# Kernel optimization log

Hardware: AMD Instinct MI355X
Metric: run time of the kernel (lower is better)

## Reference

```python
import jax, jax.numpy as jnp
import numpy as np

NHEADS = 16
NGROUPS = 16
NEG = -1e9

def _apply_rope(t, cos, sin):
    # t: (B,T,H,hs) -> pairs (B,T,H,hs//2,2); complex multiply by (cos + i*sin)
    B, T, H, hs = t.shape
    tp = t.reshape(B, T, H, hs // 2, 2)
    a, b = tp[..., 0], tp[..., 1]
    c = cos[None, :, None, :]
    s = sin[None, :, None, :]
    out = jnp.stack([a * c - b * s, a * s + b * c], axis=-1)
    return out.reshape(B, T, H, hs)

def _causal_attn(q, k, v):
    # q,k: (..., S, d); v: (..., S, dv); causal softmax attention, scale 1/sqrt(d)
    d = q.shape[-1]
    S = q.shape[-2]
    scores = jnp.einsum('...qd,...kd->...qk', q, k) / jnp.sqrt(jnp.asarray(d, q.dtype))
    mask = jnp.tril(jnp.ones((S, S), dtype=bool))
    scores = jnp.where(mask, scores, NEG)
    p = jax.nn.softmax(scores, axis=-1)
    return jnp.einsum('...qk,...kd->...qd', p, v)

def setup_inputs() -> dict:
    key = jax.random.key(0)
    k1, k2, k3 = jax.random.split(key, 3)
    B, T, C = 4, 2048, 1024
    hs = C // NHEADS
    x = jax.random.normal(k1, (B, T, C), dtype=jnp.float32)
    w_attn = jax.random.normal(k2, (3 * C, C), dtype=jnp.float32) * (1.0 / np.sqrt(C))
    w_proj = jax.random.normal(k3, (C, C), dtype=jnp.float32) * (1.0 / np.sqrt(C))
    # standard RoPE frequencies: theta_i = 10000^{-2i/hs}
    inv = 1.0 / (10000.0 ** (np.arange(0, hs, 2, dtype=np.float32) / hs))  # (hs//2,)
    ang = np.arange(T, dtype=np.float32)[:, None] * inv[None, :]           # (T, hs//2)
    freqs_cos = jnp.asarray(np.cos(ang), dtype=jnp.float32)
    freqs_sin = jnp.asarray(np.sin(ang), dtype=jnp.float32)
    return {'x': x, 'w_attn': w_attn, 'w_proj': w_proj,
            'freqs_cos': freqs_cos, 'freqs_sin': freqs_sin}

def reference(x, w_attn, w_proj, freqs_cos, freqs_sin):
    B, T, C = x.shape
    H = NHEADS
    hs = C // H
    G = min(T // (T // NGROUPS), NGROUPS)  # group_t = block_size // ngroups, T == block_size
    Tg = T // G
    qkv = x @ w_attn.T                      # (B,T,3C)
    q, k, v = jnp.split(qkv, 3, axis=2)
    # RoPE
    q = _apply_rope(q.reshape(B, T, H, hs), freqs_cos, freqs_sin).reshape(B, T, C)
    k = _apply_rope(k.reshape(B, T, H, hs), freqs_cos, freqs_sin).reshape(B, T, C)
    # group: (B, G, Tg, H, hs) -> (B, H, G, Tg, hs)
    def grp(t):
        return t.reshape(B, G, Tg, H, hs).transpose(0, 3, 1, 2, 4)
    q, k, v = grp(q), grp(k), grp(v)
    # its_time branch: append mean-pooled summary token per group
    q = jnp.concatenate([q, q.mean(axis=3, keepdims=True)], axis=3)  # (B,H,G,Tg+1,hs)
    k = jnp.concatenate([k, k.mean(axis=3, keepdims=True)], axis=3)
    v = jnp.concatenate([v, v.mean(axis=3, keepdims=True)], axis=3)
    att = _causal_attn(q, k, v)             # (B,H,G,Tg+1,hs)
    # group-level attention over summary tokens of all but last group
    q2 = q[:, :, :-1, -1]                   # (B,H,G-1,hs)
    k2 = k[:, :, :-1, -1]
    av = att[:, :, :-1, -1]                 # (B,H,G-1,hs)
    v2 = _causal_attn(q2, k2, av)           # (B,H,G-1,hs)
    y_q = q2[:, :, :, None, :]              # (B,H,G-1,1,hs)
    y_k = k2[:, :, :, None, :]
    y_v = v2[:, :, :, None, :]
    # drop summary tokens, merge groups back: (B,H,G,Tg,hs) -> (B,T,C)
    xo = att[:, :, :, :-1]
    xo = xo.reshape(B, H, T, hs).transpose(0, 2, 1, 3).reshape(B, T, C)
    out = xo @ w_proj.T
    return (out, y_q, y_k, y_v)
```

## Files before the change

kernel.cpp:

```cpp
#include <hip/hip_runtime.h>
#include <hip/hip_bf16.h>

#define HS 64
#define NH 16
#define NG 16
#define TT 2048
#define CC 1024
#define BBATCH 4
#define TG 128
#define SS 129

typedef __attribute__((ext_vector_type(8))) short bf16x8;
typedef __attribute__((ext_vector_type(4))) float f32x4;

__device__ __forceinline__ float bf2f(ushort u) {
  return __uint_as_float(((unsigned)u) << 16);
}
__device__ __forceinline__ ushort f2bf(float f) {
  unsigned x = __float_as_uint(f);
  x += 0x7fff + ((x >> 16) & 1);
  return (ushort)(x >> 16);
}
__device__ __forceinline__ bf16x8 mk8(ushort4 a0, ushort4 a1) {
  bf16x8 v;
  v[0] = (short)a0.x; v[1] = (short)a0.y; v[2] = (short)a0.z; v[3] = (short)a0.w;
  v[4] = (short)a1.x; v[5] = (short)a1.y; v[6] = (short)a1.z; v[7] = (short)a1.w;
  return v;
}

__global__ void cvt3(const float* __restrict__ x, const float* __restrict__ wa,
                     const float* __restrict__ wp, ushort* __restrict__ xb,
                     ushort* __restrict__ wab, ushort* __restrict__ wpb) {
  const int stride = gridDim.x * blockDim.x;
  for (int i = blockIdx.x * blockDim.x + threadIdx.x; i < 3145728; i += stride) {
    const float* src; ushort* dst; int off;
    if (i < 2097152) { src = x; dst = xb; off = i; }
    else if (i < 2883584) { src = wa; dst = wab; off = i - 2097152; }
    else { src = wp; dst = wpb; off = i - 2883584; }
    float4 v = ((const float4*)src)[off];
    ushort4 o;
    o.x = f2bf(v.x); o.y = f2bf(v.y); o.z = f2bf(v.z); o.w = f2bf(v.w);
    ((ushort4*)dst)[off] = o;
  }
}

__global__ __launch_bounds__(512) void gemm_qkv3(const ushort* __restrict__ A,
                                                 const ushort* __restrict__ Bw,
                                                 ushort* __restrict__ Cout) {
  const int Kd = 1024, Nd = 3072;
  __shared__ ushort As[128][68];
  __shared__ ushort Bs[384][68];
  const int m0 = blockIdx.y * 128;
  const int n0 = blockIdx.x * 384;
  const int tid = threadIdx.x;
  const int lane = tid & 63;
  const int wv = tid >> 6;
  const int wm = wv >> 2, wn = wv & 3;
  const int lo = lane & 15, hi = lane >> 4;
  const int rb = tid >> 3;
  const int c8 = (tid & 7) * 8;

  f32x4 acc[4][6];
#pragma unroll
  for (int i = 0; i < 4; ++i)
#pragma unroll
    for (int j = 0; j < 6; ++j) acc[i][j] = (f32x4)0.0f;

  uint4 v0, v1, v2, v3, v4, v5, v6, v7;
#define LOADQ(k0_)                                                              \
  {                                                                             \
    v0 = *(const uint4*)(A + (size_t)(m0 + rb) * Kd + (k0_) + c8);              \
    v1 = *(const uint4*)(A + (size_t)(m0 + rb + 64) * Kd + (k0_) + c8);         \
    v2 = *(const uint4*)(Bw + (size_t)(n0 + rb) * Kd + (k0_) + c8);             \
    v3 = *(const uint4*)(Bw + (size_t)(n0 + rb + 64) * Kd + (k0_) + c8);        \
    v4 = *(const uint4*)(Bw + (size_t)(n0 + rb + 128) * Kd + (k0_) + c8);       \
    v5 = *(const uint4*)(Bw + (size_t)(n0 + rb + 192) * Kd + (k0_) + c8);       \
    v6 = *(const uint4*)(Bw + (size_t)(n0 + rb + 256) * Kd + (k0_) + c8);       \
    v7 = *(const uint4*)(Bw + (size_t)(n0 + rb + 320) * Kd + (k0_) + c8);       \
  }
#define STOREQ                                                                  \
  {                                                                             \
    *(uint2*)&As[rb][c8]            = make_uint2(v0.x, v0.y);                   \
    *(uint2*)&As[rb][c8 + 4]        = make_uint2(v0.z, v0.w);                   \
    *(uint2*)&As[rb + 64][c8]       = make_uint2(v1.x, v1.y);                   \
    *(uint2*)&As[rb + 64][c8 + 4]   = make_uint2(v1.z, v1.w);                   \
    *(uint2*)&Bs[rb][c8]            = make_uint2(v2.x, v2.y);                   \
    *(uint2*)&Bs[rb][c8 + 4]        = make_uint2(v2.z, v2.w);                   \
    *(uint2*)&Bs[rb + 64][c8]       = make_uint2(v3.x, v3.y);                   \
    *(uint2*)&Bs[rb + 64][c8 + 4]   = make_uint2(v3.z, v3.w);                   \
    *(uint2*)&Bs[rb + 128][c8]      = make_uint2(v4.x, v4.y);                   \
    *(uint2*)&Bs[rb + 128][c8 + 4]  = make_uint2(v4.z, v4.w);                   \
    *(uint2*)&Bs[rb + 192][c8]      = make_uint2(v5.x, v5.y);                   \
    *(uint2*)&Bs[rb + 192][c8 + 4]  = make_uint2(v5.z, v5.w);                   \
    *(uint2*)&Bs[rb + 256][c8]      = make_uint2(v6.x, v6.y);                   \
    *(uint2*)&Bs[rb + 256][c8 + 4]  = make_uint2(v6.z, v6.w);                   \
    *(uint2*)&Bs[rb + 320][c8]      = make_uint2(v7.x, v7.y);                   \
    *(uint2*)&Bs[rb + 320][c8 + 4]  = make_uint2(v7.z, v7.w);                   \
  }

  LOADQ(0)
  for (int t = 0; t < 16; ++t) {
    __syncthreads();
    STOREQ
    __syncthreads();
    if (t < 15) LOADQ((t + 1) * 64)
#pragma unroll
    for (int kk = 0; kk < 64; kk += 32) {
      bf16x8 af[4], bfr[6];
#pragma unroll
      for (int i = 0; i < 4; ++i) {
        int r = wm * 64 + i * 16 + lo;
        af[i] = mk8(*(const ushort4*)&As[r][kk + 4 * hi],
                    *(const ushort4*)&As[r][kk + 16 + 4 * hi]);
      }
#pragma unroll
      for (int j = 0; j < 6; ++j) {
        int r = wn * 96 + j * 16 + lo;
        bfr[j] = mk8(*(const ushort4*)&Bs[r][kk + 4 * hi],
                     *(const ushort4*)&Bs[r][kk + 16 + 4 * hi]);
      }
#pragma unroll
      for (int i = 0; i < 4; ++i)
#pragma unroll
        for (int j = 0; j < 6; ++j)
          acc[i][j] = __builtin_amdgcn_mfma_f32_16x16x32_bf16(af[i], bfr[j], acc[i][j], 0, 0, 0);
    }
  }
#undef LOADQ
#undef STOREQ

#pragma unroll
  for (int i = 0; i < 4; ++i) {
    int row = m0 + wm * 64 + i * 16 + 4 * hi;
#pragma unroll
    for (int j = 0; j < 6; ++j) {
      int col = n0 + wn * 96 + j * 16 + lo;
#pragma unroll
      for (int r = 0; r < 4; ++r)
        Cout[(size_t)(row + r) * Nd + col] = f2bf(acc[i][j][r]);
    }
  }
}

template <bool OUT_BF16>
__global__ __launch_bounds__(256) void gemm_bt(const ushort* __restrict__ A,
                                               const ushort* __restrict__ Bw,
                                               void* __restrict__ Cout,
                                               int M, int N, int K) {
  __shared__ ushort As[128][68];
  __shared__ ushort Bs[128][68];
  const int m0 = blockIdx.y * 128;
  const int n0 = blockIdx.x * 128;
  const int tid = threadIdx.x;
  const int lane = tid & 63;
  const int wv = tid >> 6;
  const int wr = wv >> 1, wc = wv & 1;
  const int lo = lane & 15, hi = lane >> 4;

  f32x4 acc[4][4];
#pragma unroll
  for (int i = 0; i < 4; ++i)
#pragma unroll
    for (int j = 0; j < 4; ++j) acc[i][j] = (f32x4)0.0f;

  for (int k0 = 0; k0 < K; k0 += 64) {
    __syncthreads();
#pragma unroll
    for (int t = 0; t < 4; ++t) {
      int c = tid + 256 * t;
      int row = c >> 3, cc = c & 7;
      uint4 va = *(const uint4*)(A + (size_t)(m0 + row) * K + k0 + cc * 8);
      *(uint2*)&As[row][cc * 8]     = make_uint2(va.x, va.y);
      *(uint2*)&As[row][cc * 8 + 4] = make_uint2(va.z, va.w);
      uint4 vb = *(const uint4*)(Bw + (size_t)(n0 + row) * K + k0 + cc * 8);
      *(uint2*)&Bs[row][cc * 8]     = make_uint2(vb.x, vb.y);
      *(uint2*)&Bs[row][cc * 8 + 4] = make_uint2(vb.z, vb.w);
    }
    __syncthreads();
#pragma unroll
    for (int kk = 0; kk < 64; kk += 32) {
      bf16x8 af[4], bfr[4];
#pragma unroll
      for (int i = 0; i < 4; ++i) {
        int r = wr * 64 + i * 16 + lo;
        af[i] = mk8(*(const ushort4*)&As[r][kk + 4 * hi],
                    *(const ushort4*)&As[r][kk + 16 + 4 * hi]);
      }
#pragma unroll
      for (int j = 0; j < 4; ++j) {
        int r = wc * 64 + j * 16 + lo;
        bfr[j] = mk8(*(const ushort4*)&Bs[r][kk + 4 * hi],
                     *(const ushort4*)&Bs[r][kk + 16 + 4 * hi]);
      }
#pragma unroll
      for (int i = 0; i < 4; ++i)
#pragma unroll
        for (int j = 0; j < 4; ++j)
          acc[i][j] = __builtin_amdgcn_mfma_f32_16x16x32_bf16(af[i], bfr[j], acc[i][j], 0, 0, 0);
    }
  }
#pragma unroll
  for (int i = 0; i < 4; ++i) {
    int row = m0 + wr * 64 + i * 16 + 4 * hi;
#pragma unroll
    for (int j = 0; j < 4; ++j) {
      int col = n0 + wc * 64 + j * 16 + lo;
#pragma unroll
      for (int r = 0; r < 4; ++r) {
        float v = acc[i][j][r];
        if constexpr (OUT_BF16) {
          ((ushort*)Cout)[(size_t)(row + r) * N + col] = f2bf(v);
        } else {
          ((float*)Cout)[(size_t)(row + r) * N + col] = v;
        }
      }
    }
  }
}

__global__ __launch_bounds__(512, 4) void attn1f(const ushort* __restrict__ qkv,
                                                 const float* __restrict__ fc,
                                                 const float* __restrict__ fs,
                                                 ushort* __restrict__ xo, float* __restrict__ attm,
                                                 float* __restrict__ yq, float* __restrict__ yk) {
  __shared__ ushort qs[144][68];
  __shared__ ushort ks[144][68];
  __shared__ ushort vt[64][148];
  __shared__ ushort obuf[8][16][68];
  float (*redL)[8][24] = reinterpret_cast<float(*)[8][24]>(&obuf[0][0][0]);
  const int blk = blockIdx.x;
  const int g = blk & 15, h = (blk >> 4) & 15, b = blk >> 8;
  const int tid = threadIdx.x;
  const int lane = tid & 63, wv = tid >> 6;
  const int lo = lane & 15, hi = lane >> 4;

  if (tid < 320) {
    int d = tid / 5, ch = (tid % 5) * 4;
    *(ushort4*)&vt[d][128 + ch] = make_ushort4(0, 0, 0, 0);
  }

  const size_t rowbase = (size_t)(b * TT + g * TG) * (3 * CC) + h * HS;
  const int srow = tid >> 3;
  const int c8 = (tid & 7) * 8;
  float msq[8], msk[8], msv[8];
#pragma unroll
  for (int j = 0; j < 8; ++j) { msq[j] = 0.f; msk[j] = 0.f; msv[j] = 0.f; }
#pragma unroll
  for (int it = 0; it < 6; ++it) {
    const int part = it >> 1;
    const int s = srow + 64 * (it & 1);
    uint4 w = *(const uint4*)(qkv + rowbase + (size_t)s * (3 * CC) + part * CC + c8);
    ushort e[8];
    *(uint4*)e = w;
    if (part == 2) {
#pragma unroll
      for (int j = 0; j < 8; ++j) { msv[j] += bf2f(e[j]); vt[c8 + j][s] = e[j]; }
    } else {
      const int ts = g * TG + s;
      float4 cv = *(const float4*)&fc[ts * 32 + (c8 >> 1)];
      float4 sv = *(const float4*)&fs[ts * 32 + (c8 >> 1)];
      float a0 = bf2f(e[0]), a1 = bf2f(e[1]), a2 = bf2f(e[2]), a3 = bf2f(e[3]);
      float a4 = bf2f(e[4]), a5 = bf2f(e[5]), a6 = bf2f(e[6]), a7 = bf2f(e[7]);
      float r0 = a0 * cv.x - a1 * sv.x, r1 = a0 * sv.x + a1 * cv.x;
      float r2 = a2 * cv.y - a3 * sv.y, r3 = a2 * sv.y + a3 * cv.y;
      float r4 = a4 * cv.z - a5 * sv.z, r5 = a4 * sv.z + a5 * cv.z;
      float r6 = a6 * cv.w - a7 * sv.w, r7 = a6 * sv.w + a7 * cv.w;
      uint4 o;
      o.x = (unsigned)f2bf(r0) | ((unsigned)f2bf(r1) << 16);
      o.y = (unsigned)f2bf(r2) | ((unsigned)f2bf(r3) << 16);
      o.z = (unsigned)f2bf(r4) | ((unsigned)f2bf(r5) << 16);
      o.w = (unsigned)f2bf(r6) | ((unsigned)f2bf(r7) << 16);
      if (part == 0) {
        *(uint4*)&qs[s][c8] = o;
        msq[0] += r0; msq[1] += r1; msq[2] += r2; msq[3] += r3;
        msq[4] += r4; msq[5] += r5; msq[6] += r6; msq[7] += r7;
      } else {
        *(uint4*)&ks[s][c8] = o;
        msk[0] += r0; msk[1] += r1; msk[2] += r2; msk[3] += r3;
        msk[4] += r4; msk[5] += r5; msk[6] += r6; msk[7] += r7;
      }
    }
  }
#pragma unroll
  for (int j = 0; j < 8; ++j) {
    msq[j] += __shfl_xor(msq[j], 8); msq[j] += __shfl_xor(msq[j], 16); msq[j] += __shfl_xor(msq[j], 32);
    msk[j] += __shfl_xor(msk[j], 8); msk[j] += __shfl_xor(msk[j], 16); msk[j] += __shfl_xor(msk[j], 32);
    msv[j] += __shfl_xor(msv[j], 8); msv[j] += __shfl_xor(msv[j], 16); msv[j] += __shfl_xor(msv[j], 32);
  }
  if (lane < 8) {
#pragma unroll
    for (int j = 0; j < 8; ++j) {
      redL[wv][lane][j] = msq[j];
      redL[wv][lane][8 + j] = msk[j];
      redL[wv][lane][16 + j] = msv[j];
    }
  }
  __syncthreads();
  if (tid < 64) {
    const int cg = tid >> 3, j = tid & 7;
    float mq = 0.f, mk2 = 0.f, mv = 0.f;
#pragma unroll
    for (int w = 0; w < 8; ++w) {
      mq += redL[w][cg][j];
      mk2 += redL[w][cg][8 + j];
      mv += redL[w][cg][16 + j];
    }
    mq *= (1.0f / 128.0f); mk2 *= (1.0f / 128.0f); mv *= (1.0f / 128.0f);
    qs[128][tid] = f2bf(mq);
    ks[128][tid] = f2bf(mk2);
    vt[tid][128] = f2bf(mv);
    if (g < 15) {
      size_t yo = ((size_t)(b * 16 + h) * 15 + g) * 64 + tid;
      yq[yo] = mq; yk[yo] = mk2;
    }
  }
  __syncthreads();

#pragma unroll
  for (int ti = 0; ti < 2; ++ti) {
    const int t = (ti == 0) ? (8 - wv) : ((wv == 7) ? 0 : -1);
    if (t < 0) continue;
    const int q0 = t * 16;

    bf16x8 bq[2];
#pragma unroll
    for (int k2 = 0; k2 < 2; ++k2)
      bq[k2] = mk8(*(const ushort4*)&qs[q0 + lo][k2 * 32 + 4 * hi],
                   *(const ushort4*)&qs[q0 + lo][k2 * 32 + 16 + 4 * hi]);

    f32x4 sc[9];
#pragma unroll
    for (int n = 0; n < 9; ++n) sc[n] = (f32x4)0.0f;
#pragma unroll
    for (int n = 0; n < 9; ++n) {
      if (n > t) continue;
#pragma unroll
      for (int k2 = 0; k2 < 2; ++k2) {
        bf16x8 ak = mk8(*(const ushort4*)&ks[n * 16 + lo][k2 * 32 + 4 * hi],
                        *(const ushort4*)&ks[n * 16 + lo][k2 * 32 + 16 + 4 * hi]);
        sc[n] = __builtin_amdgcn_mfma_f32_16x16x32_bf16(ak, bq[k2], sc[n], 0, 0, 0);
      }
    }

    const int qi = q0 + lo;
    float mx = -INFINITY;
#pragma unroll
    for (int n = 0; n < 9; ++n) {
      if (n > t) continue;
#pragma unroll
      for (int r = 0; r < 4; ++r) {
        int kj = n * 16 + 4 * hi + r;
        float v = (kj <= qi) ? sc[n][r] * 0.125f : -INFINITY;
        sc[n][r] = v;
        mx = fmaxf(mx, v);
      }
    }
    mx = fmaxf(mx, __shfl_xor(mx, 16));
    mx = fmaxf(mx, __shfl_xor(mx, 32));
    float sum = 0.f;
#pragma unroll
    for (int n = 0; n < 9; ++n) {
      if (n > t) continue;
#pragma unroll
      for (int r = 0; r < 4; ++r) {
        float e = __expf(sc[n][r] - mx);
        sc[n][r] = e;
        sum += e;
      }
    }
    sum += __shfl_xor(sum, 16);
    sum += __shfl_xor(sum, 32);
    const float inv = 1.0f / sum;

    f32x4 oac[4];
#pragma unroll
    for (int m = 0; m < 4; ++m) oac[m] = (f32x4)0.0f;
#pragma unroll
    for (int s2 = 0; s2 < 5; ++s2) {
      if (s2 > (t >> 1)) continue;
      const int kt1ok = (2 * s2 + 1 <= t);
      bf16x8 pb;
#pragma unroll
      for (int e = 0; e < 4; ++e) pb[e] = (short)f2bf(sc[2 * s2][e] * inv);
      if (kt1ok) {
#pragma unroll
        for (int e = 0; e < 4; ++e) pb[e + 4] = (short)f2bf(sc[2 * s2 + 1][e] * inv);
      } else {
#pragma unroll
        for (int e = 0; e < 4; ++e) pb[e + 4] = 0;
      }
#pragma unroll
      for (int m = 0; m < 4; ++m) {
        ushort4 a0 = *(const ushort4*)&vt[m * 16 + lo][32 * s2 + 4 * hi];
        ushort4 a1 = kt1ok ? *(const ushort4*)&vt[m * 16 + lo][32 * s2 + 16 + 4 * hi]
                           : make_ushort4(0, 0, 0, 0);
        oac[m] = __builtin_amdgcn_mfma_f32_16x16x32_bf16(mk8(a0, a1), pb, oac[m], 0, 0, 0);
      }
    }

    if (t < 8) {
#pragma unroll
      for (int m = 0; m < 4; ++m)
#pragma unroll
        for (int r = 0; r < 4; ++r)
          obuf[wv][lo][m * 16 + 4 * hi + r] = f2bf(oac[m][r]);
#pragma unroll
      for (int it = 0; it < 4; ++it) {
        int idx = lane + 64 * it;
        int r = idx >> 4;
        int c4 = (idx & 15) * 4;
        uint2 val = *(const uint2*)&obuf[wv][r][c4];
        int tok = g * TG + t * 16 + r;
        *(uint2*)(xo + ((size_t)(b * TT + tok)) * CC + h * HS + c4) = val;
      }
    } else {
      if (lo == 0) {
#pragma unroll
        for (int m = 0; m < 4; ++m)
#pragma unroll
          for (int r = 0; r < 4; ++r)
            attm[(size_t)blk * 64 + m * 16 + 4 * hi + r] = oac[m][r];
      }
    }
  }
}

__global__ __launch_bounds__(64) void attn2(const float* __restrict__ yq,
                                            const float* __restrict__ yk,
                                            const float* __restrict__ attm,
                                            float* __restrict__ yv) {
  __shared__ float qs2[15][64], ks2[15][64], avs[15][64], srow[16];
  int bh = blockIdx.x, lane = threadIdx.x;
  for (int j = 0; j < 15; ++j) {
    qs2[j][lane] = yq[((size_t)bh * 15 + j) * 64 + lane];
    ks2[j][lane] = yk[((size_t)bh * 15 + j) * 64 + lane];
    avs[j][lane] = attm[((size_t)bh * 16 + j) * 64 + lane];
  }
  __syncthreads();
  for (int i = 0; i < 15; ++i) {
    float qv = qs2[i][lane];
    for (int j = 0; j <= i; ++j) {
      float t = qv * ks2[j][lane];
#pragma unroll
      for (int off = 32; off > 0; off >>= 1) t += __shfl_xor(t, off);
      if (lane == 0) srow[j] = t * 0.125f;
    }
    __syncthreads();
    float mx = -INFINITY;
    for (int j = 0; j <= i; ++j) mx = fmaxf(mx, srow[j]);
    float den = 0;
    for (int j = 0; j <= i; ++j) den += __expf(srow[j] - mx);
    float inv = 1.0f / den;
    float o = 0;
    for (int j = 0; j <= i; ++j) o += __expf(srow[j] - mx) * inv * avs[j][lane];
    yv[((size_t)bh * 15 + i) * 64 + lane] = o;
    __syncthreads();
  }
}

extern "C" void kernel_launch(void* const* d_in, const int* in_sizes, int n_in,
                              void* d_out, int out_size, void* d_ws, size_t ws_size,
                              hipStream_t stream) {
  const float* x      = (const float*)d_in[0];
  const float* w_attn = (const float*)d_in[1];
  const float* w_proj = (const float*)d_in[2];
  const float* fc     = (const float*)d_in[3];
  const float* fs     = (const float*)d_in[4];
  float* out = (float*)d_out;

  char* ws = (char*)d_ws;
  ushort* xb   = (ushort*)(ws);
  ushort* xo   = (ushort*)(ws);
  ushort* wab  = (ushort*)(ws + 16777216);
  float*  attm = (float*) (ws + 16777216);
  ushort* wpb  = (ushort*)(ws + 23068672);
  ushort* qkv  = (ushort*)(ws + 25165824);

  float* yq = out + 8388608;
  float* yk = out + 8450048;
  float* yv = out + 8511488;

  cvt3<<<2048, 256, 0, stream>>>(x, w_attn, w_proj, xb, wab, wpb);
  gemm_qkv3<<<dim3(8, 64), 512, 0, stream>>>(xb, wab, qkv);
  attn1f<<<1024, 512, 0, stream>>>(qkv, fc, fs, xo, attm, yq, yk);
  attn2<<<64, 64, 0, stream>>>(yq, yk, attm, yv);
  gemm_bt<false><<<dim3(8, 64), 256, 0, stream>>>(xo, wpb, out, 8192, 1024, 1024);
}
```

Baseline: 179.5 us.

## Drop Q and output LDS buffers in attn1f to raise occupancy

The q shared tile is removed: each wave re-reads its own query rows from global qkv and applies RoPE in registers right before the QK MFMA. Only the mean summary row stays in a small shared buffer. The output staging buffer is also removed, so results go straight from accumulators to global memory as ushort4 stores. The V padding is reduced and the launch-bounds occupancy hint rises from 4 to 6 blocks. The aim is to cut LDS use per block so more blocks fit per CU, at the cost of a second global read of Q with RoPE recomputed and less coalesced output writes.

```diff
diff --git a/kernel.cpp b/kernel.cpp
--- a/kernel.cpp
+++ b/kernel.cpp
@@ -218,25 +218,24 @@
   }
 }
 
-__global__ __launch_bounds__(512, 4) void attn1f(const ushort* __restrict__ qkv,
+__global__ __launch_bounds__(512, 6) void attn1f(const ushort* __restrict__ qkv,
                                                  const float* __restrict__ fc,
                                                  const float* __restrict__ fs,
                                                  ushort* __restrict__ xo, float* __restrict__ attm,
                                                  float* __restrict__ yq, float* __restrict__ yk) {
-  __shared__ ushort qs[144][68];
   __shared__ ushort ks[144][68];
-  __shared__ ushort vt[64][148];
-  __shared__ ushort obuf[8][16][68];
-  float (*redL)[8][24] = reinterpret_cast<float(*)[8][24]>(&obuf[0][0][0]);
+  __shared__ ushort vt[64][144];
+  __shared__ float redL[8][8][24];
+  __shared__ ushort mqrow[64];
   const int blk = blockIdx.x;
   const int g = blk & 15, h = (blk >> 4) & 15, b = blk >> 8;
   const int tid = threadIdx.x;
   const int lane = tid & 63, wv = tid >> 6;
   const int lo = lane & 15, hi = lane >> 4;
 
-  if (tid < 320) {
-    int d = tid / 5, ch = (tid % 5) * 4;
-    *(ushort4*)&vt[d][128 + ch] = make_ushort4(0, 0, 0, 0);
+  if (tid < 256) {
+    int d = tid >> 2, c4 = 128 + (tid & 3) * 4;
+    *(ushort4*)&vt[d][c4] = make_ushort4(0, 0, 0, 0);
   }
 
   const size_t rowbase = (size_t)(b * TT + g * TG) * (3 * CC) + h * HS;
@@ -265,16 +264,15 @@
       float r2 = a2 * cv.y - a3 * sv.y, r3 = a2 * sv.y + a3 * cv.y;
       float r4 = a4 * cv.z - a5 * sv.z, r5 = a4 * sv.z + a5 * cv.z;
       float r6 = a6 * cv.w - a7 * sv.w, r7 = a6 * sv.w + a7 * cv.w;
-      uint4 o;
-      o.x = (unsigned)f2bf(r0) | ((unsigned)f2bf(r1) << 16);
-      o.y = (unsigned)f2bf(r2) | ((unsigned)f2bf(r3) << 16);
-      o.z = (unsigned)f2bf(r4) | ((unsigned)f2bf(r5) << 16);
-      o.w = (unsigned)f2bf(r6) | ((unsigned)f2bf(r7) << 16);
       if (part == 0) {
-        *(uint4*)&qs[s][c8] = o;
         msq[0] += r0; msq[1] += r1; msq[2] += r2; msq[3] += r3;
         msq[4] += r4; msq[5] += r5; msq[6] += r6; msq[7] += r7;
       } else {
+        uint4 o;
+        o.x = (unsigned)f2bf(r0) | ((unsigned)f2bf(r1) << 16);
+        o.y = (unsigned)f2bf(r2) | ((unsigned)f2bf(r3) << 16);
+        o.z = (unsigned)f2bf(r4) | ((unsigned)f2bf(r5) << 16);
+        o.w = (unsigned)f2bf(r6) | ((unsigned)f2bf(r7) << 16);
         *(uint4*)&ks[s][c8] = o;
         msk[0] += r0; msk[1] += r1; msk[2] += r2; msk[3] += r3;
         msk[4] += r4; msk[5] += r5; msk[6] += r6; msk[7] += r7;
@@ -306,7 +304,7 @@
       mv += redL[w][cg][16 + j];
     }
     mq *= (1.0f / 128.0f); mk2 *= (1.0f / 128.0f); mv *= (1.0f / 128.0f);
-    qs[128][tid] = f2bf(mq);
+    mqrow[tid] = f2bf(mq);
     ks[128][tid] = f2bf(mk2);
     vt[tid][128] = f2bf(mv);
     if (g < 15) {
@@ -323,10 +321,39 @@
     const int q0 = t * 16;
 
     bf16x8 bq[2];
-#pragma unroll
-    for (int k2 = 0; k2 < 2; ++k2)
-      bq[k2] = mk8(*(const ushort4*)&qs[q0 + lo][k2 * 32 + 4 * hi],
-                   *(const ushort4*)&qs[q0 + lo][k2 * 32 + 16 + 4 * hi]);
+    if (t < 8) {
+      const ushort* qrow = qkv + rowbase + (size_t)(q0 + lo) * (3 * CC);
+      const int ts = g * TG + q0 + lo;
+#pragma unroll
+      for (int k2 = 0; k2 < 2; ++k2) {
+        ushort4 u0 = *(const ushort4*)(qrow + k2 * 32 + 4 * hi);
+        ushort4 u1 = *(const ushort4*)(qrow + k2 * 32 + 16 + 4 * hi);
+        const int pidx = ts * 32 + k2 * 16 + 2 * hi;
+        float2 c0 = *(const float2*)&fc[pidx], s0 = *(const float2*)&fs[pidx];
+        float2 c1 = *(const float2*)&fc[pidx + 8], s1 = *(const float2*)&fs[pidx + 8];
+        float q0f = bf2f(u0.x), q1f = bf2f(u0.y), q2f = bf2f(u0.z), q3f = bf2f(u0.w);
+        float q4f = bf2f(u1.x), q5f = bf2f(u1.y), q6f = bf2f(u1.z), q7f = bf2f(u1.w);
+        bf16x8 v;
+        v[0] = (short)f2bf(q0f * c0.x - q1f * s0.x);
+        v[1] = (short)f2bf(q0f * s0.x + q1f * c0.x);
+        v[2] = (short)f2bf(q2f * c0.y - q3f * s0.y);
+        v[3] = (short)f2bf(q2f * s0.y + q3f * c0.y);
+        v[4] = (short)f2bf(q4f * c1.x - q5f * s1.x);
+        v[5] = (short)f2bf(q4f * s1.x + q5f * c1.x);
+        v[6] = (short)f2bf(q6f * c1.y - q7f * s1.y);
+        v[7] = (short)f2bf(q6f * s1.y + q7f * c1.y);
+        bq[k2] = v;
+      }
+    } else {
+#pragma unroll
+      for (int k2 = 0; k2 < 2; ++k2) {
+        ushort4 a0 = *(const ushort4*)&mqrow[k2 * 32 + 4 * hi];
+        ushort4 a1 = *(const ushort4*)&mqrow[k2 * 32 + 16 + 4 * hi];
+        bf16x8 v = mk8(a0, a1);
+        if (lo != 0) v = (bf16x8)(short)0;
+        bq[k2] = v;
+      }
+    }
 
     f32x4 sc[9];
 #pragma unroll
@@ -399,19 +426,13 @@
     }
 
     if (t < 8) {
-#pragma unroll
-      for (int m = 0; m < 4; ++m)
-#pragma unroll
-        for (int r = 0; r < 4; ++r)
-          obuf[wv][lo][m * 16 + 4 * hi + r] = f2bf(oac[m][r]);
-#pragma unroll
-      for (int it = 0; it < 4; ++it) {
-        int idx = lane + 64 * it;
-        int r = idx >> 4;
-        int c4 = (idx & 15) * 4;
-        uint2 val = *(const uint2*)&obuf[wv][r][c4];
-        int tok = g * TG + t * 16 + r;
-        *(uint2*)(xo + ((size_t)(b * TT + tok)) * CC + h * HS + c4) = val;
+      ushort* xrow = xo + ((size_t)(b * TT + g * TG + q0 + lo)) * CC + h * HS + 4 * hi;
+#pragma unroll
+      for (int m = 0; m < 4; ++m) {
+        ushort4 o4;
+        o4.x = f2bf(oac[m][0]); o4.y = f2bf(oac[m][1]);
+        o4.z = f2bf(oac[m][2]); o4.w = f2bf(oac[m][3]);
+        *(ushort4*)(xrow + m * 16) = o4;
       }
     } else {
       if (lo == 0) {
```

After: 187.8 us. +4.7%, slower.

## Widen projection GEMM tile to 128x256 with register-prefetched global loads

Applied to the files above, without the earlier changes.

Replaces the generic 128x128 output-projection GEMM with a specialized kernel using 512 threads and a 128x256 tile, cutting the grid from 512 to 256 blocks. It prefetches the next K-slice from global memory into registers while the current slice is being multiplied, overlapping load latency with MFMA work. The cost is more registers and shared memory per block and fewer blocks, which may leave some CUs idle on a large-CU device.

```diff
diff --git a/kernel.cpp b/kernel.cpp
--- a/kernel.cpp
+++ b/kernel.cpp
@@ -142,20 +142,21 @@
   }
 }
 
-template <bool OUT_BF16>
-__global__ __launch_bounds__(256) void gemm_bt(const ushort* __restrict__ A,
-                                               const ushort* __restrict__ Bw,
-                                               void* __restrict__ Cout,
-                                               int M, int N, int K) {
+__global__ __launch_bounds__(512) void gemm_proj2(const ushort* __restrict__ A,
+                                                  const ushort* __restrict__ Bw,
+                                                  float* __restrict__ Cout) {
+  const int Kd = 1024, Nd = 1024;
   __shared__ ushort As[128][68];
-  __shared__ ushort Bs[128][68];
+  __shared__ ushort Bs[256][68];
   const int m0 = blockIdx.y * 128;
-  const int n0 = blockIdx.x * 128;
+  const int n0 = blockIdx.x * 256;
   const int tid = threadIdx.x;
   const int lane = tid & 63;
   const int wv = tid >> 6;
-  const int wr = wv >> 1, wc = wv & 1;
+  const int wm = wv >> 2, wn = wv & 3;
   const int lo = lane & 15, hi = lane >> 4;
+  const int rb = tid >> 3;
+  const int c8 = (tid & 7) * 8;
 
   f32x4 acc[4][4];
 #pragma unroll
@@ -163,32 +164,50 @@
 #pragma unroll
     for (int j = 0; j < 4; ++j) acc[i][j] = (f32x4)0.0f;
 
-  for (int k0 = 0; k0 < K; k0 += 64) {
+  uint4 v0, v1, v2, v3, v4, v5;
+#define LOADP(k0_)                                                              \
+  {                                                                             \
+    v0 = *(const uint4*)(A + (size_t)(m0 + rb) * Kd + (k0_) + c8);              \
+    v1 = *(const uint4*)(A + (size_t)(m0 + rb + 64) * Kd + (k0_) + c8);         \
+    v2 = *(const uint4*)(Bw + (size_t)(n0 + rb) * Kd + (k0_) + c8);             \
+    v3 = *(const uint4*)(Bw + (size_t)(n0 + rb + 64) * Kd + (k0_) + c8);        \
+    v4 = *(const uint4*)(Bw + (size_t)(n0 + rb + 128) * Kd + (k0_) + c8);       \
+    v5 = *(const uint4*)(Bw + (size_t)(n0 + rb + 192) * Kd + (k0_) + c8);       \
+  }
+#define STOREP                                                                  \
+  {                                                                             \
+    *(uint2*)&As[rb][c8]            = make_uint2(v0.x, v0.y);                   \
+    *(uint2*)&As[rb][c8 + 4]        = make_uint2(v0.z, v0.w);                   \
+    *(uint2*)&As[rb + 64][c8]       = make_uint2(v1.x, v1.y);                   \
+    *(uint2*)&As[rb + 64][c8 + 4]   = make_uint2(v1.z, v1.w);                   \
+    *(uint2*)&Bs[rb][c8]            = make_uint2(v2.x, v2.y);                   \
+    *(uint2*)&Bs[rb][c8 + 4]        = make_uint2(v2.z, v2.w);                   \
+    *(uint2*)&Bs[rb + 64][c8]       = make_uint2(v3.x, v3.y);                   \
+    *(uint2*)&Bs[rb + 64][c8 + 4]   = make_uint2(v3.z, v3.w);                   \
+    *(uint2*)&Bs[rb + 128][c8]      = make_uint2(v4.x, v4.y);                   \
+    *(uint2*)&Bs[rb + 128][c8 + 4]  = make_uint2(v4.z, v4.w);                   \
+    *(uint2*)&Bs[rb + 192][c8]      = make_uint2(v5.x, v5.y);                   \
+    *(uint2*)&Bs[rb + 192][c8 + 4]  = make_uint2(v5.z, v5.w);                   \
+  }
+
+  LOADP(0)
+  for (int t = 0; t < 16; ++t) {
     __syncthreads();
-#pragma unroll
-    for (int t = 0; t < 4; ++t) {
-      int c = tid + 256 * t;
-      int row = c >> 3, cc = c & 7;
-      uint4 va = *(const uint4*)(A + (size_t)(m0 + row) * K + k0 + cc * 8);
-      *(uint2*)&As[row][cc * 8]     = make_uint2(va.x, va.y);
-      *(uint2*)&As[row][cc * 8 + 4] = make_uint2(va.z, va.w);
-      uint4 vb = *(const uint4*)(Bw + (size_t)(n0 + row) * K + k0 + cc * 8);
-      *(uint2*)&Bs[row][cc * 8]     = make_uint2(vb.x, vb.y);
-      *(uint2*)&Bs[row][cc * 8 + 4] = make_uint2(vb.z, vb.w);
-    }
+    STOREP
     __syncthreads();
+    if (t < 15) LOADP((t + 1) * 64)
 #pragma unroll
     for (int kk = 0; kk < 64; kk += 32) {
       bf16x8 af[4], bfr[4];
 #pragma unroll
       for (int i = 0; i < 4; ++i) {
-        int r = wr * 64 + i * 16 + lo;
+        int r = wm * 64 + i * 16 + lo;
         af[i] = mk8(*(const ushort4*)&As[r][kk + 4 * hi],
                     *(const ushort4*)&As[r][kk + 16 + 4 * hi]);
       }
 #pragma unroll
       for (int j = 0; j < 4; ++j) {
-        int r = wc * 64 + j * 16 + lo;
+        int r = wn * 64 + j * 16 + lo;
         bfr[j] = mk8(*(const ushort4*)&Bs[r][kk + 4 * hi],
                      *(const ushort4*)&Bs[r][kk + 16 + 4 * hi]);
       }
@@ -199,21 +218,18 @@
           acc[i][j] = __builtin_amdgcn_mfma_f32_16x16x32_bf16(af[i], bfr[j], acc[i][j], 0, 0, 0);
     }
   }
+#undef LOADP
+#undef STOREP
+
 #pragma unroll
   for (int i = 0; i < 4; ++i) {
-    int row = m0 + wr * 64 + i * 16 + 4 * hi;
+    int row = m0 + wm * 64 + i * 16 + 4 * hi;
 #pragma unroll
     for (int j = 0; j < 4; ++j) {
-      int col = n0 + wc * 64 + j * 16 + lo;
-#pragma unroll
-      for (int r = 0; r < 4; ++r) {
-        float v = acc[i][j][r];
-        if constexpr (OUT_BF16) {
-          ((ushort*)Cout)[(size_t)(row + r) * N + col] = f2bf(v);
-        } else {
-          ((float*)Cout)[(size_t)(row + r) * N + col] = v;
-        }
-      }
+      int col = n0 + wn * 64 + j * 16 + lo;
+#pragma unroll
+      for (int r = 0; r < 4; ++r)
+        Cout[(size_t)(row + r) * Nd + col] = acc[i][j][r];
     }
   }
 }
@@ -484,5 +500,5 @@
   gemm_qkv3<<<dim3(8, 64), 512, 0, stream>>>(xb, wab, qkv);
   attn1f<<<1024, 512, 0, stream>>>(qkv, fc, fs, xo, attm, yq, yk);
   attn2<<<64, 64, 0, stream>>>(yq, yk, attm, yv);
-  gemm_bt<false><<<dim3(8, 64), 256, 0, stream>>>(xo, wpb, out, 8192, 1024, 1024);
-}
+  gemm_proj2<<<dim3(4, 64), 512, 0, stream>>>(xo, wpb, out);
+}
```

Result: no change. 178.8 us (-0.4%).
